# Kernel optimization log

Hardware: AMD Instinct MI355X
Metric: run time of the kernel (lower is better)

## Reference

```python
import math
import jax, jax.numpy as jnp
import numpy as np

EMBED_DIM = 1024
N_HEADS = 16
HEAD_DIM = EMBED_DIM // N_HEADS
B, T = 4, 2048


def setup_inputs() -> dict:
    key = jax.random.key(0)
    k1, k2, k3 = jax.random.split(key, 3)
    scale_in = 1.0 / math.sqrt(EMBED_DIM)
    return {
        "x": jax.random.normal(k1, (B, T, EMBED_DIM), dtype=jnp.float32),
        "direction": 0,  # 0=FORWARD (causal), 1=RETRODICTION (anti-causal), 2=CORRECTION (causal)
        "qkv_w": jax.random.normal(k2, (EMBED_DIM, 3 * EMBED_DIM), dtype=jnp.float32) * scale_in,
        "qkv_b": jnp.zeros((3 * EMBED_DIM,), dtype=jnp.float32),
        "proj_w": jax.random.normal(k3, (EMBED_DIM, EMBED_DIM), dtype=jnp.float32) * scale_in,
        "proj_b": jnp.zeros((EMBED_DIM,), dtype=jnp.float32),
    }


def reference(x, direction, qkv_w, qkv_b, proj_w, proj_b):
    Bx, Tx, C = x.shape
    qkv = x @ qkv_w + qkv_b                        # [B,T,3C]
    q, k, v = jnp.split(qkv, 3, axis=-1)
    # [B,T,C] -> [B,H,T,D]
    def heads(t):
        return t.reshape(Bx, Tx, N_HEADS, HEAD_DIM).transpose(0, 2, 1, 3)
    q, k, v = heads(q), heads(k), heads(v)
    scale = 1.0 / math.sqrt(HEAD_DIM)
    attn = jnp.einsum('bhqd,bhkd->bhqk', q, k) * scale
    rows = jnp.arange(Tx)[:, None]
    cols = jnp.arange(Tx)[None, :]
    if direction == 1:  # RETRODICTION -> anti-causal (upper triangular allowed)
        mask = cols >= rows
    else:               # FORWARD / CORRECTION -> causal
        mask = cols <= rows
    attn = jnp.where(mask[None, None], attn, -jnp.inf)
    attn = jax.nn.softmax(attn, axis=-1)  # dropout p=0 -> identity
    out = jnp.einsum('bhqk,bhkd->bhqd', attn, v)   # [B,H,T,D]
    out = out.transpose(0, 2, 1, 3).reshape(Bx, Tx, C)
    return out @ proj_w + proj_b
```

## Files before the change

### kernel.cpp

```cpp
#include <hip/hip_runtime.h>
#include <math.h>

typedef __bf16 bf16_t;
typedef bf16_t bf16x8 __attribute__((ext_vector_type(8)));
typedef bf16_t bf16x4 __attribute__((ext_vector_type(4)));
typedef float  f32x4  __attribute__((ext_vector_type(4)));
typedef float  floatv4 __attribute__((ext_vector_type(4)));

#define AS1 __attribute__((address_space(1)))
#define AS3 __attribute__((address_space(3)))

static __device__ __forceinline__ void gld_lds16(const void* g, void* l) {
  __builtin_amdgcn_global_load_lds((const AS1 unsigned int*)g,
                                   (AS3 unsigned int*)l, 16, 0, 0);
}
static __device__ __forceinline__ void block_sync() {
  asm volatile("" ::: "memory");
  __builtin_amdgcn_s_barrier();
  asm volatile("" ::: "memory");
}

__global__ __launch_bounds__(256) void k_cast(const float* __restrict__ in,
                                              bf16_t* __restrict__ out, int n4) {
  int i = blockIdx.x * 256 + threadIdx.x;
  if (i >= n4) return;
  floatv4 v = ((const floatv4*)in)[i];
  bf16x4 o;
  o.x = (bf16_t)v.x; o.y = (bf16_t)v.y; o.z = (bf16_t)v.z; o.w = (bf16_t)v.w;
  ((bf16x4*)out)[i] = o;
}

__global__ __launch_bounds__(256) void k_transpose_cast(const float* __restrict__ in,
                                                        bf16_t* __restrict__ out,
                                                        int R, int Cc) {
  __shared__ float tile[32][33];
  int c0 = blockIdx.x * 32, r0 = blockIdx.y * 32;
  int tx = threadIdx.x, ty = threadIdx.y;
#pragma unroll
  for (int i = 0; i < 32; i += 8)
    tile[ty + i][tx] = in[(size_t)(r0 + ty + i) * Cc + c0 + tx];
  __syncthreads();
#pragma unroll
  for (int i = 0; i < 32; i += 8)
    out[(size_t)(c0 + ty + i) * R + r0 + tx] = (bf16_t)tile[tx][ty + i];
}

__global__ __launch_bounds__(512, 2) void k_gemm_qkv(
    const bf16_t* __restrict__ A, const bf16_t* __restrict__ Bt,
    const float* __restrict__ bias,
    bf16_t* __restrict__ qo, bf16_t* __restrict__ ko, bf16_t* __restrict__ vto) {
  const int K = 1024;
  __shared__ __align__(16) char smem[122880];
  const int m0 = blockIdx.x * 256, n0 = blockIdx.y * 384;
  const int t = threadIdx.x, lane = t & 63, wv = t >> 6;
  const int ln15 = lane & 15, lhi = lane >> 4;
  const int wr = wv >> 2, wc = wv & 3;

  f32x4 acc[8][6];
#pragma unroll
  for (int m = 0; m < 8; ++m)
#pragma unroll
    for (int n = 0; n < 6; ++n) acc[m][n] = (f32x4){0.f, 0.f, 0.f, 0.f};
  bf16x8 af[4], bfr[6];

  const bf16_t* aS = A + (size_t)(m0 + wv * 16 + ln15) * K + lhi * 8;
  const bf16_t* bS = Bt + (size_t)(n0 + wv * 16 + ln15) * K + lhi * 8;
  const int dA = wv * 1024 + lane * 16;

  auto stageA = [&](int k0, char* buf) {
    gld_lds16(aS + k0, buf + dA);
    gld_lds16(aS + (size_t)128 * K + k0, buf + 8192 + dA);
  };
  auto stageB = [&](int k0, char* buf) {
    gld_lds16(bS + k0, buf + 16384 + dA);
    gld_lds16(bS + (size_t)128 * K + k0, buf + 24576 + dA);
    gld_lds16(bS + (size_t)256 * K + k0, buf + 32768 + dA);
  };

  char* b0 = smem;
  char* b1 = smem + 40960;
  char* b2 = smem + 81920;
  stageA(0, b0); stageB(0, b0);
  stageA(32, b1); stageB(32, b1);
  asm volatile("s_waitcnt vmcnt(5)" ::: "memory");
  block_sync();

#pragma unroll 1
  for (int it = 0; it < 32; ++it) {
    const bool st = (it + 2 < 32);
    const int k0n = (it + 2) * 32;
#pragma unroll
    for (int m = 0; m < 4; ++m)
      af[m] = *(const bf16x8*)(b0 + (wr * 8 + m) * 1024 + lane * 16);
#pragma unroll
    for (int n = 0; n < 6; ++n)
      bfr[n] = *(const bf16x8*)(b0 + 16384 + (wc * 6 + n) * 1024 + lane * 16);
    if (st) stageA(k0n, b2);
    block_sync();
    asm volatile("s_waitcnt lgkmcnt(0)" ::: "memory");
    __builtin_amdgcn_sched_barrier(0);
    __builtin_amdgcn_s_setprio(1);
#pragma unroll
    for (int m = 0; m < 4; ++m)
#pragma unroll
      for (int n = 0; n < 6; ++n)
        acc[m][n] = __builtin_amdgcn_mfma_f32_16x16x32_bf16(af[m], bfr[n], acc[m][n], 0, 0, 0);
    __builtin_amdgcn_s_setprio(0);
    block_sync();
#pragma unroll
    for (int m = 0; m < 4; ++m)
      af[m] = *(const bf16x8*)(b0 + (wr * 8 + 4 + m) * 1024 + lane * 16);
    if (st) stageB(k0n, b2);
    block_sync();
    asm volatile("s_waitcnt lgkmcnt(0)" ::: "memory");
    __builtin_amdgcn_sched_barrier(0);
    __builtin_amdgcn_s_setprio(1);
#pragma unroll
    for (int m = 0; m < 4; ++m)
#pragma unroll
      for (int n = 0; n < 6; ++n)
        acc[4 + m][n] = __builtin_amdgcn_mfma_f32_16x16x32_bf16(af[m], bfr[n], acc[4 + m][n], 0, 0, 0);
    __builtin_amdgcn_s_setprio(0);
    if (st) asm volatile("s_waitcnt vmcnt(5)" ::: "memory");
    else if (it + 1 < 32) asm volatile("s_waitcnt vmcnt(0)" ::: "memory");
    block_sync();
    char* tmp = b0; b0 = b1; b1 = b2; b2 = tmp;
  }

  bf16_t* L = (bf16_t*)smem;
  const int bq = m0 >> 11, ttb = m0 & 2047;
#pragma unroll 1
  for (int p = 0; p < 3; ++p) {
    const int wcol0 = n0 + p * 128;
    const int which = wcol0 >> 10;
    const float bscale = (which == 0) ? 0.18033688011112042f : 1.0f;
#pragma unroll
    for (int n = 0; n < 6; ++n) {
      const int c16 = wc * 6 + n;
      if ((c16 >> 3) == p) {
        const int colL = c16 * 16 - p * 128 + ln15;
        const float bv = bias[n0 + c16 * 16 + ln15];
#pragma unroll
        for (int m = 0; m < 8; ++m)
#pragma unroll
          for (int j = 0; j < 4; ++j) {
            const int row = wr * 128 + m * 16 + lhi * 4 + j;
            const bf16_t ob = (bf16_t)((acc[m][n][j] + bv) * bscale);
            if (which == 2) L[colL * 264 + row] = ob;
            else            L[row * 132 + colL] = ob;
          }
      }
    }
    block_sync();
    if (which == 2) {
#pragma unroll
      for (int c = 0; c < 8; ++c) {
        const int idx = c * 512 + t;
        const int vcol = idx >> 5, r8 = (idx & 31) * 8;
        bf16x8 v8 = *(const bf16x8*)&L[vcol * 264 + r8];
        const int cc = (wcol0 & 1023) + vcol;
        const int hh = cc >> 6, d = cc & 63;
        *(bf16x8*)&vto[((size_t)(bq * 16 + hh) * 64 + d) * 2048 + ttb + r8] = v8;
      }
    } else {
      bf16_t* dst = (which == 0) ? qo : ko;
#pragma unroll
      for (int c = 0; c < 8; ++c) {
        const int idx = c * 512 + t;
        const int row = idx >> 4, c8 = (idx & 15) * 8;
        bf16x8 v8 = *(const bf16x8*)&L[row * 132 + c8];
        const int cc = (wcol0 & 1023) + c8;
        const int hh = cc >> 6, d = cc & 63;
        *(bf16x8*)&dst[((size_t)(bq * 16 + hh) * 2048 + ttb + row) * 64 + d] = v8;
      }
    }
    block_sync();
  }
}

__global__ __launch_bounds__(256) void k_attn4(
    const bf16_t* __restrict__ q, const bf16_t* __restrict__ k,
    const bf16_t* __restrict__ vt, const int* __restrict__ dirp,
    bf16_t* __restrict__ a2) {
  const int T = 2048;
  __shared__ __align__(16) bf16_t smem[16384];
  const int bh = blockIdx.x, b = bh >> 4, h = bh & 15;
  const int jb = blockIdx.y;
  const int t = threadIdx.x, lane = t & 63, wv = t >> 6;
  const int ln15 = lane & 15, lhi = lane >> 4;
  const bool anti = (*dirp == 1);

  const bf16_t* kbase = k + (size_t)bh * T * 64;
  const bf16_t* vbase = vt + (size_t)bh * 64 * T;

  auto stage = [&](int kc0, int buf) {
    char* Kd = (char*)smem + buf * 16384;
    char* Vd = Kd + 8192;
#pragma unroll
    for (int s = 0; s < 2; ++s) {
      const int qk = s * 4 + wv;
      const int krow = kc0 + (qk >> 2) * 32 + ((qk >> 1) & 1) * 4 +
                       ((lane & 15) >> 2) * 8 + (lane & 3);
      const int kcolb = (lane >> 4) * 16 + (qk & 1) * 64;
      gld_lds16((const char*)kbase + (size_t)krow * 128 + kcolb,
                Kd + s * 4096 + t * 16);
      const int vd = (qk & 3) * 16 + (lane & 15);
      gld_lds16((const char*)vbase + (size_t)vd * 4096 + (size_t)kc0 * 2 +
                    (qk >> 2) * 64 + (lane >> 4) * 16,
                Vd + s * 4096 + t * 16);
    }
  };

#pragma unroll 1
  for (int sel = 0; sel < 2; ++sel) {
    const int qt = sel ? (15 - jb) : jb;
    const int q0w = qt * 128 + wv * 32;

    bf16x8 qf[2][2];
#pragma unroll
    for (int g = 0; g < 2; ++g) {
      const bf16_t* qp = q + ((size_t)bh * T + q0w + g * 16 + ln15) * 64 + lhi * 8;
      qf[g][0] = *(const bf16x8*)qp;
      qf[g][1] = *(const bf16x8*)(qp + 32);
    }

    f32x4 acc[2][4];
#pragma unroll
    for (int g = 0; g < 2; ++g)
#pragma unroll
      for (int dg = 0; dg < 4; ++dg) acc[g][dg] = (f32x4){0.f, 0.f, 0.f, 0.f};
    float mrun[2] = {-3.0e38f, -3.0e38f}, lrun[2] = {0.f, 0.f};

    const int kt0 = anti ? 2 * qt : 0;
    const int nb  = anti ? (32 - 2 * qt) : (2 * qt + 2);

    stage(kt0 * 64, 0);
#pragma unroll 1
    for (int i = 0; i < nb; ++i) {
      const int kt = kt0 + i;
      const int buf = i & 1;
      if (i + 1 < nb) {
        stage((kt + 1) * 64, buf ^ 1);
        asm volatile("s_waitcnt vmcnt(4)" ::: "memory");
      } else {
        asm volatile("s_waitcnt vmcnt(0)" ::: "memory");
      }
      block_sync();
      const bf16_t* Kb = smem + buf * 8192;
      const bf16_t* Vb = Kb + 4096;

      const bool active = anti ? (kt * 64 + 63 >= q0w) : (kt * 64 <= q0w + 31);
      if (active) {
        float sc[2][16];
#pragma unroll
        for (int kh = 0; kh < 2; ++kh) {
          bf16x8 kf0 = *(const bf16x8*)(Kb + (kh * 4 + 0) * 512 + lane * 8);
          bf16x8 kf1 = *(const bf16x8*)(Kb + (kh * 4 + 1) * 512 + lane * 8);
          bf16x8 kf2 = *(const bf16x8*)(Kb + (kh * 4 + 2) * 512 + lane * 8);
          bf16x8 kf3 = *(const bf16x8*)(Kb + (kh * 4 + 3) * 512 + lane * 8);
#pragma unroll
          for (int g = 0; g < 2; ++g) {
            const f32x4 zz = (f32x4){0.f, 0.f, 0.f, 0.f};
            f32x4 slo = __builtin_amdgcn_mfma_f32_16x16x32_bf16(kf0, qf[g][0], zz, 0, 0, 0);
            slo = __builtin_amdgcn_mfma_f32_16x16x32_bf16(kf1, qf[g][1], slo, 0, 0, 0);
            f32x4 shi = __builtin_amdgcn_mfma_f32_16x16x32_bf16(kf2, qf[g][0], zz, 0, 0, 0);
            shi = __builtin_amdgcn_mfma_f32_16x16x32_bf16(kf3, qf[g][1], shi, 0, 0, 0);
#pragma unroll
            for (int j = 0; j < 4; ++j) {
              sc[g][kh * 8 + j] = slo[j];
              sc[g][kh * 8 + 4 + j] = shi[j];
            }
          }
        }
        bf16x8 vfr[8];
#pragma unroll
        for (int dg = 0; dg < 8; ++dg)
          vfr[dg] = *(const bf16x8*)(Vb + dg * 512 + lane * 8);
#pragma unroll
        for (int g = 0; g < 2; ++g) {
          const int grow = q0w + g * 16 + ln15;
          const bool needm = anti ? (kt * 64 < q0w + g * 16 + 15)
                                  : (kt * 64 + 63 > q0w + g * 16);
          if (needm) {
#pragma unroll
            for (int e = 0; e < 16; ++e) {
              const int col = kt * 64 + (e >> 3) * 32 + lhi * 8 + (e & 7);
              const bool ok = anti ? (col >= grow) : (col <= grow);
              sc[g][e] = ok ? sc[g][e] : -3.0e38f;
            }
          }
          float lmax = sc[g][0];
#pragma unroll
          for (int e = 1; e < 16; ++e) lmax = fmaxf(lmax, sc[g][e]);
          if (!__all(lmax <= mrun[g] + 8.f)) {
            float vm = lmax;
            vm = fmaxf(vm, __shfl_xor(vm, 16));
            vm = fmaxf(vm, __shfl_xor(vm, 32));
            const float mn = fmaxf(mrun[g], vm);
            const float al = __builtin_amdgcn_exp2f(mrun[g] - mn);
            lrun[g] *= al;
#pragma unroll
            for (int dg = 0; dg < 4; ++dg) acc[g][dg] *= al;
            mrun[g] = mn;
          }
          bf16x8 pb0, pb1;
          float rs = 0.f;
#pragma unroll
          for (int e = 0; e < 8; ++e) {
            float p = __builtin_amdgcn_exp2f(sc[g][e] - mrun[g]);
            rs += p; pb0[e] = (bf16_t)p;
          }
#pragma unroll
          for (int e = 0; e < 8; ++e) {
            float p = __builtin_amdgcn_exp2f(sc[g][8 + e] - mrun[g]);
            rs += p; pb1[e] = (bf16_t)p;
          }
          lrun[g] += rs;
#pragma unroll
          for (int dg = 0; dg < 4; ++dg)
            acc[g][dg] = __builtin_amdgcn_mfma_f32_16x16x32_bf16(vfr[dg], pb0, acc[g][dg], 0, 0, 0);
#pragma unroll
          for (int dg = 0; dg < 4; ++dg)
            acc[g][dg] = __builtin_amdgcn_mfma_f32_16x16x32_bf16(vfr[4 + dg], pb1, acc[g][dg], 0, 0, 0);
        }
      }
      block_sync();
    }

#pragma unroll
    for (int g = 0; g < 2; ++g) {
      float l = lrun[g];
      l += __shfl_xor(l, 16);
      l += __shfl_xor(l, 32);
      const float inv = __builtin_amdgcn_rcpf(l);
      bf16_t* op = a2 + ((size_t)b * T + q0w + g * 16 + ln15) * 1024 + h * 64 + lhi * 4;
#pragma unroll
      for (int dg = 0; dg < 4; ++dg) {
        bf16x4 o4;
#pragma unroll
        for (int jx = 0; jx < 4; ++jx) o4[jx] = (bf16_t)(acc[g][dg][jx] * inv);
        *(bf16x4*)(op + dg * 16) = o4;
      }
    }
  }
}

__global__ __launch_bounds__(512, 2) void k_gemm_proj(
    const bf16_t* __restrict__ A, const bf16_t* __restrict__ Bt,
    const float* __restrict__ bias, float* __restrict__ out) {
  const int K = 1024;
  __shared__ __align__(16) char smem[73728];
  const int m0 = blockIdx.x * 256, n0 = blockIdx.y * 128;
  const int t = threadIdx.x, lane = t & 63, wv = t >> 6;
  const int ln15 = lane & 15, lhi = lane >> 4;
  const int wr = wv >> 2, wc = wv & 3;

  f32x4 acc[8][2];
#pragma unroll
  for (int m = 0; m < 8; ++m)
#pragma unroll
    for (int n = 0; n < 2; ++n) acc[m][n] = (f32x4){0.f, 0.f, 0.f, 0.f};
  bf16x8 af[4], bfr[2];

  const bf16_t* aS = A + (size_t)(m0 + wv * 16 + ln15) * K + lhi * 8;
  const bf16_t* bS = Bt + (size_t)(n0 + wv * 16 + ln15) * K + lhi * 8;
  const int dA = wv * 1024 + lane * 16;

  auto stageA = [&](int k0, char* buf) {
    gld_lds16(aS + k0, buf + dA);
    gld_lds16(aS + (size_t)128 * K + k0, buf + 8192 + dA);
  };
  auto stageB = [&](int k0, char* buf) {
    gld_lds16(bS + k0, buf + 16384 + dA);
  };

  char* b0 = smem;
  char* b1 = smem + 24576;
  char* b2 = smem + 49152;
  stageA(0, b0); stageB(0, b0);
  stageA(32, b1); stageB(32, b1);
  asm volatile("s_waitcnt vmcnt(3)" ::: "memory");
  block_sync();

#pragma unroll 1
  for (int it = 0; it < 32; ++it) {
    const bool st = (it + 2 < 32);
    const int k0n = (it + 2) * 32;
#pragma unroll
    for (int m = 0; m < 4; ++m)
      af[m] = *(const bf16x8*)(b0 + (wr * 8 + m) * 1024 + lane * 16);
#pragma unroll
    for (int n = 0; n < 2; ++n)
      bfr[n] = *(const bf16x8*)(b0 + 16384 + (wc * 2 + n) * 1024 + lane * 16);
    if (st) stageA(k0n, b2);
    block_sync();
    asm volatile("s_waitcnt lgkmcnt(0)" ::: "memory");
    __builtin_amdgcn_sched_barrier(0);
    __builtin_amdgcn_s_setprio(1);
#pragma unroll
    for (int m = 0; m < 4; ++m)
#pragma unroll
      for (int n = 0; n < 2; ++n)
        acc[m][n] = __builtin_amdgcn_mfma_f32_16x16x32_bf16(af[m], bfr[n], acc[m][n], 0, 0, 0);
    __builtin_amdgcn_s_setprio(0);
    block_sync();
#pragma unroll
    for (int m = 0; m < 4; ++m)
      af[m] = *(const bf16x8*)(b0 + (wr * 8 + 4 + m) * 1024 + lane * 16);
    if (st) stageB(k0n, b2);
    block_sync();
    asm volatile("s_waitcnt lgkmcnt(0)" ::: "memory");
    __builtin_amdgcn_sched_barrier(0);
    __builtin_amdgcn_s_setprio(1);
#pragma unroll
    for (int m = 0; m < 4; ++m)
#pragma unroll
      for (int n = 0; n < 2; ++n)
        acc[4 + m][n] = __builtin_amdgcn_mfma_f32_16x16x32_bf16(af[m], bfr[n], acc[4 + m][n], 0, 0, 0);
    __builtin_amdgcn_s_setprio(0);
    if (st) asm volatile("s_waitcnt vmcnt(3)" ::: "memory");
    else if (it + 1 < 32) asm volatile("s_waitcnt vmcnt(0)" ::: "memory");
    block_sync();
    char* tmp = b0; b0 = b1; b1 = b2; b2 = tmp;
  }

#pragma unroll
  for (int n = 0; n < 2; ++n) {
    const int col = n0 + wc * 32 + n * 16 + ln15;
    const float bv = bias[col];
#pragma unroll
    for (int m = 0; m < 8; ++m)
#pragma unroll
      for (int j = 0; j < 4; ++j) {
        const int row = m0 + wr * 128 + m * 16 + lhi * 4 + j;
        out[(size_t)row * 1024 + col] = acc[m][n][j] + bv;
      }
  }
}

extern "C" void kernel_launch(void* const* d_in, const int* in_sizes, int n_in,
                              void* d_out, int out_size, void* d_ws, size_t ws_size,
                              hipStream_t stream) {
  (void)in_sizes; (void)n_in; (void)out_size; (void)ws_size;
  const float* x      = (const float*)d_in[0];
  const int*   dirp   = (const int*)d_in[1];
  const float* qkv_w  = (const float*)d_in[2];
  const float* qkv_b  = (const float*)d_in[3];
  const float* proj_w = (const float*)d_in[4];
  const float* proj_b = (const float*)d_in[5];
  float* out = (float*)d_out;

  char* ws = (char*)d_ws;
  bf16_t* xb   = (bf16_t*)(ws);
  bf16_t* wq_t = (bf16_t*)(ws + 16777216);
  bf16_t* wp_t = (bf16_t*)(ws + 23068672);
  bf16_t* qb   = (bf16_t*)(ws + 25165824);
  bf16_t* kb   = (bf16_t*)(ws + 41943040);
  bf16_t* vtb  = (bf16_t*)(ws + 58720256);
  bf16_t* a2   = xb;

  k_cast<<<8192, 256, 0, stream>>>(x, xb, 2097152);
  k_transpose_cast<<<dim3(96, 32), dim3(32, 8), 0, stream>>>(qkv_w, wq_t, 1024, 3072);
  k_transpose_cast<<<dim3(32, 32), dim3(32, 8), 0, stream>>>(proj_w, wp_t, 1024, 1024);
  k_gemm_qkv<<<dim3(32, 8), 512, 0, stream>>>(xb, wq_t, qkv_b, qb, kb, vtb);
  k_attn4<<<dim3(64, 8), 256, 0, stream>>>(qb, kb, vtb, dirp, a2);
  k_gemm_proj<<<dim3(32, 8), 512, 0, stream>>>(a2, wp_t, proj_b, out);
}
```

Measured before the change: 193.1 us.

## Replace LDS-staged GEMM pipelines with direct global-to-register double-buffered MFMA loops

Both the QKV and output-projection GEMMs drop their LDS-staged, triple-buffered pipelines and their barrier-heavy main loops. Each wave now loads its A and B fragments straight from global memory into registers, double-buffered, and computes a 64x64 subtile. The QKV GEMM tile shrinks from 256x384 to 256x128, which triples the grid and simplifies the epilogue to a single output pass. The goal is to remove barrier and LDS overhead and to raise parallelism, at the cost of relying on L1/L2 caches for reuse across waves and of less coalesced strided global loads.

Result: slower. 332.0 us (+71.9%).

```diff
diff --git a/kernel.cpp b/kernel.cpp
--- a/kernel.cpp
+++ b/kernel.cpp
@@ -50,131 +50,87 @@
     const float* __restrict__ bias,
     bf16_t* __restrict__ qo, bf16_t* __restrict__ ko, bf16_t* __restrict__ vto) {
   const int K = 1024;
-  __shared__ __align__(16) char smem[122880];
-  const int m0 = blockIdx.x * 256, n0 = blockIdx.y * 384;
+  __shared__ __align__(16) char smem[67584];
+  const int m0 = blockIdx.x * 256, n0 = blockIdx.y * 128;
   const int t = threadIdx.x, lane = t & 63, wv = t >> 6;
   const int ln15 = lane & 15, lhi = lane >> 4;
-  const int wr = wv >> 2, wc = wv & 3;
-
-  f32x4 acc[8][6];
-#pragma unroll
-  for (int m = 0; m < 8; ++m)
-#pragma unroll
-    for (int n = 0; n < 6; ++n) acc[m][n] = (f32x4){0.f, 0.f, 0.f, 0.f};
-  bf16x8 af[4], bfr[6];
-
-  const bf16_t* aS = A + (size_t)(m0 + wv * 16 + ln15) * K + lhi * 8;
-  const bf16_t* bS = Bt + (size_t)(n0 + wv * 16 + ln15) * K + lhi * 8;
-  const int dA = wv * 1024 + lane * 16;
-
-  auto stageA = [&](int k0, char* buf) {
-    gld_lds16(aS + k0, buf + dA);
-    gld_lds16(aS + (size_t)128 * K + k0, buf + 8192 + dA);
-  };
-  auto stageB = [&](int k0, char* buf) {
-    gld_lds16(bS + k0, buf + 16384 + dA);
-    gld_lds16(bS + (size_t)128 * K + k0, buf + 24576 + dA);
-    gld_lds16(bS + (size_t)256 * K + k0, buf + 32768 + dA);
-  };
-
-  char* b0 = smem;
-  char* b1 = smem + 40960;
-  char* b2 = smem + 81920;
-  stageA(0, b0); stageB(0, b0);
-  stageA(32, b1); stageB(32, b1);
-  asm volatile("s_waitcnt vmcnt(5)" ::: "memory");
+  const int wr = wv >> 1, wc = wv & 1;
+
+  f32x4 acc[4][4];
+#pragma unroll
+  for (int m = 0; m < 4; ++m)
+#pragma unroll
+    for (int n = 0; n < 4; ++n) acc[m][n] = (f32x4){0.f, 0.f, 0.f, 0.f};
+
+  const bf16_t* aP = A + (size_t)(m0 + wr * 64 + ln15) * K + lhi * 8;
+  const bf16_t* bP = Bt + (size_t)(n0 + wc * 64 + ln15) * K + lhi * 8;
+
+  auto LD = [&](bf16x8 af[4], bf16x8 bf[4], int k0) {
+#pragma unroll
+    for (int m = 0; m < 4; ++m)
+      af[m] = *(const bf16x8*)(aP + (size_t)m * 16 * K + k0);
+#pragma unroll
+    for (int n = 0; n < 4; ++n)
+      bf[n] = *(const bf16x8*)(bP + (size_t)n * 16 * K + k0);
+  };
+  auto FM = [&](const bf16x8 af[4], const bf16x8 bf[4]) {
+#pragma unroll
+    for (int m = 0; m < 4; ++m)
+#pragma unroll
+      for (int n = 0; n < 4; ++n)
+        acc[m][n] = __builtin_amdgcn_mfma_f32_16x16x32_bf16(af[m], bf[n], acc[m][n], 0, 0, 0);
+  };
+
+  bf16x8 a0[4], b0[4], a1[4], b1[4];
+  LD(a0, b0, 0);
+#pragma unroll 1
+  for (int k0 = 0; k0 < K; k0 += 64) {
+    LD(a1, b1, k0 + 32);
+    FM(a0, b0);
+    if (k0 + 64 < K) LD(a0, b0, k0 + 64);
+    FM(a1, b1);
+  }
+
+  const int which = n0 >> 10;
+  const float bscale = (which == 0) ? 0.18033688011112042f : 1.0f;
+  bf16_t* L = (bf16_t*)smem;
+#pragma unroll
+  for (int n = 0; n < 4; ++n) {
+    const int col = wc * 64 + n * 16 + ln15;
+    const float bv = bias[n0 + col];
+#pragma unroll
+    for (int m = 0; m < 4; ++m)
+#pragma unroll
+      for (int j = 0; j < 4; ++j) {
+        const int row = wr * 64 + m * 16 + lhi * 4 + j;
+        const bf16_t ob = (bf16_t)((acc[m][n][j] + bv) * bscale);
+        if (which == 2) L[col * 264 + row] = ob;
+        else            L[row * 132 + col] = ob;
+      }
+  }
   block_sync();
-
-#pragma unroll 1
-  for (int it = 0; it < 32; ++it) {
-    const bool st = (it + 2 < 32);
-    const int k0n = (it + 2) * 32;
-#pragma unroll
-    for (int m = 0; m < 4; ++m)
-      af[m] = *(const bf16x8*)(b0 + (wr * 8 + m) * 1024 + lane * 16);
-#pragma unroll
-    for (int n = 0; n < 6; ++n)
-      bfr[n] = *(const bf16x8*)(b0 + 16384 + (wc * 6 + n) * 1024 + lane * 16);
-    if (st) stageA(k0n, b2);
-    block_sync();
-    asm volatile("s_waitcnt lgkmcnt(0)" ::: "memory");
-    __builtin_amdgcn_sched_barrier(0);
-    __builtin_amdgcn_s_setprio(1);
-#pragma unroll
-    for (int m = 0; m < 4; ++m)
-#pragma unroll
-      for (int n = 0; n < 6; ++n)
-        acc[m][n] = __builtin_amdgcn_mfma_f32_16x16x32_bf16(af[m], bfr[n], acc[m][n], 0, 0, 0);
-    __builtin_amdgcn_s_setprio(0);
-    block_sync();
-#pragma unroll
-    for (int m = 0; m < 4; ++m)
-      af[m] = *(const bf16x8*)(b0 + (wr * 8 + 4 + m) * 1024 + lane * 16);
-    if (st) stageB(k0n, b2);
-    block_sync();
-    asm volatile("s_waitcnt lgkmcnt(0)" ::: "memory");
-    __builtin_amdgcn_sched_barrier(0);
-    __builtin_amdgcn_s_setprio(1);
-#pragma unroll
-    for (int m = 0; m < 4; ++m)
-#pragma unroll
-      for (int n = 0; n < 6; ++n)
-        acc[4 + m][n] = __builtin_amdgcn_mfma_f32_16x16x32_bf16(af[m], bfr[n], acc[4 + m][n], 0, 0, 0);
-    __builtin_amdgcn_s_setprio(0);
-    if (st) asm volatile("s_waitcnt vmcnt(5)" ::: "memory");
-    else if (it + 1 < 32) asm volatile("s_waitcnt vmcnt(0)" ::: "memory");
-    block_sync();
-    char* tmp = b0; b0 = b1; b1 = b2; b2 = tmp;
-  }
-
-  bf16_t* L = (bf16_t*)smem;
   const int bq = m0 >> 11, ttb = m0 & 2047;
-#pragma unroll 1
-  for (int p = 0; p < 3; ++p) {
-    const int wcol0 = n0 + p * 128;
-    const int which = wcol0 >> 10;
-    const float bscale = (which == 0) ? 0.18033688011112042f : 1.0f;
-#pragma unroll
-    for (int n = 0; n < 6; ++n) {
-      const int c16 = wc * 6 + n;
-      if ((c16 >> 3) == p) {
-        const int colL = c16 * 16 - p * 128 + ln15;
-        const float bv = bias[n0 + c16 * 16 + ln15];
-#pragma unroll
-        for (int m = 0; m < 8; ++m)
-#pragma unroll
-          for (int j = 0; j < 4; ++j) {
-            const int row = wr * 128 + m * 16 + lhi * 4 + j;
-            const bf16_t ob = (bf16_t)((acc[m][n][j] + bv) * bscale);
-            if (which == 2) L[colL * 264 + row] = ob;
-            else            L[row * 132 + colL] = ob;
-          }
-      }
-    }
-    block_sync();
-    if (which == 2) {
-#pragma unroll
-      for (int c = 0; c < 8; ++c) {
-        const int idx = c * 512 + t;
-        const int vcol = idx >> 5, r8 = (idx & 31) * 8;
-        bf16x8 v8 = *(const bf16x8*)&L[vcol * 264 + r8];
-        const int cc = (wcol0 & 1023) + vcol;
-        const int hh = cc >> 6, d = cc & 63;
-        *(bf16x8*)&vto[((size_t)(bq * 16 + hh) * 64 + d) * 2048 + ttb + r8] = v8;
-      }
-    } else {
-      bf16_t* dst = (which == 0) ? qo : ko;
-#pragma unroll
-      for (int c = 0; c < 8; ++c) {
-        const int idx = c * 512 + t;
-        const int row = idx >> 4, c8 = (idx & 15) * 8;
-        bf16x8 v8 = *(const bf16x8*)&L[row * 132 + c8];
-        const int cc = (wcol0 & 1023) + c8;
-        const int hh = cc >> 6, d = cc & 63;
-        *(bf16x8*)&dst[((size_t)(bq * 16 + hh) * 2048 + ttb + row) * 64 + d] = v8;
-      }
-    }
-    block_sync();
+  if (which == 2) {
+#pragma unroll
+    for (int c = 0; c < 8; ++c) {
+      const int idx = c * 512 + t;
+      const int vcol = idx >> 5, r8 = (idx & 31) * 8;
+      bf16x8 v8 = *(const bf16x8*)&L[vcol * 264 + r8];
+      const int cc = (n0 + vcol) & 1023;
+      const int hh = cc >> 6, d = cc & 63;
+      *(bf16x8*)&vto[((size_t)(bq * 16 + hh) * 64 + d) * 2048 + ttb + r8] = v8;
+    }
+  } else {
+    bf16_t* dst = (which == 0) ? qo : ko;
+#pragma unroll
+    for (int c = 0; c < 8; ++c) {
+      const int idx = c * 512 + t;
+      const int row = idx >> 4, c8 = (idx & 15) * 8;
+      bf16x8 v8 = *(const bf16x8*)&L[row * 132 + c8];
+      const int cc = (n0 & 1023) + c8;
+      const int hh = cc >> 6, d = cc & 63;
+      *(bf16x8*)&dst[((size_t)(bq * 16 + hh) * 2048 + ttb + row) * 64 + d] = v8;
+    }
   }
 }
 
@@ -349,90 +305,55 @@
     const bf16_t* __restrict__ A, const bf16_t* __restrict__ Bt,
     const float* __restrict__ bias, float* __restrict__ out) {
   const int K = 1024;
-  __shared__ __align__(16) char smem[73728];
   const int m0 = blockIdx.x * 256, n0 = blockIdx.y * 128;
   const int t = threadIdx.x, lane = t & 63, wv = t >> 6;
   const int ln15 = lane & 15, lhi = lane >> 4;
-  const int wr = wv >> 2, wc = wv & 3;
-
-  f32x4 acc[8][2];
-#pragma unroll
-  for (int m = 0; m < 8; ++m)
-#pragma unroll
-    for (int n = 0; n < 2; ++n) acc[m][n] = (f32x4){0.f, 0.f, 0.f, 0.f};
-  bf16x8 af[4], bfr[2];
-
-  const bf16_t* aS = A + (size_t)(m0 + wv * 16 + ln15) * K + lhi * 8;
-  const bf16_t* bS = Bt + (size_t)(n0 + wv * 16 + ln15) * K + lhi * 8;
-  const int dA = wv * 1024 + lane * 16;
-
-  auto stageA = [&](int k0, char* buf) {
-    gld_lds16(aS + k0, buf + dA);
-    gld_lds16(aS + (size_t)128 * K + k0, buf + 8192 + dA);
-  };
-  auto stageB = [&](int k0, char* buf) {
-    gld_lds16(bS + k0, buf + 16384 + dA);
-  };
-
-  char* b0 = smem;
-  char* b1 = smem + 24576;
-  char* b2 = smem + 49152;
-  stageA(0, b0); stageB(0, b0);
-  stageA(32, b1); stageB(32, b1);
-  asm volatile("s_waitcnt vmcnt(3)" ::: "memory");
-  block_sync();
-
+  const int wr = wv >> 1, wc = wv & 1;
+
+  f32x4 acc[4][4];
+#pragma unroll
+  for (int m = 0; m < 4; ++m)
+#pragma unroll
+    for (int n = 0; n < 4; ++n) acc[m][n] = (f32x4){0.f, 0.f, 0.f, 0.f};
+
+  const bf16_t* aP = A + (size_t)(m0 + wr * 64 + ln15) * K + lhi * 8;
+  const bf16_t* bP = Bt + (size_t)(n0 + wc * 64 + ln15) * K + lhi * 8;
+
+  auto LD = [&](bf16x8 af[4], bf16x8 bf[4], int k0) {
+#pragma unroll
+    for (int m = 0; m < 4; ++m)
+      af[m] = *(const bf16x8*)(aP + (size_t)m * 16 * K + k0);
+#pragma unroll
+    for (int n = 0; n < 4; ++n)
+      bf[n] = *(const bf16x8*)(bP + (size_t)n * 16 * K + k0);
+  };
+  auto FM = [&](const bf16x8 af[4], const bf16x8 bf[4]) {
+#pragma unroll
+    for (int m = 0; m < 4; ++m)
+#pragma unroll
+      for (int n = 0; n < 4; ++n)
+        acc[m][n] = __builtin_amdgcn_mfma_f32_16x16x32_bf16(af[m], bf[n], acc[m][n], 0, 0, 0);
+  };
+
+  bf16x8 a0[4], b0[4], a1[4], b1[4];
+  LD(a0, b0, 0);
 #pragma unroll 1
-  for (int it = 0; it < 32; ++it) {
-    const bool st = (it + 2 < 32);
-    const int k0n = (it + 2) * 32;
-#pragma unroll
-    for (int m = 0; m < 4; ++m)
-      af[m] = *(const bf16x8*)(b0 + (wr * 8 + m) * 1024 + lane * 16);
-#pragma unroll
-    for (int n = 0; n < 2; ++n)
-      bfr[n] = *(const bf16x8*)(b0 + 16384 + (wc * 2 + n) * 1024 + lane * 16);
-    if (st) stageA(k0n, b2);
-    block_sync();
-    asm volatile("s_waitcnt lgkmcnt(0)" ::: "memory");
-    __builtin_amdgcn_sched_barrier(0);
-    __builtin_amdgcn_s_setprio(1);
-#pragma unroll
-    for (int m = 0; m < 4; ++m)
-#pragma unroll
-      for (int n = 0; n < 2; ++n)
-        acc[m][n] = __builtin_amdgcn_mfma_f32_16x16x32_bf16(af[m], bfr[n], acc[m][n], 0, 0, 0);
-    __builtin_amdgcn_s_setprio(0);
-    block_sync();
-#pragma unroll
-    for (int m = 0; m < 4; ++m)
-      af[m] = *(const bf16x8*)(b0 + (wr * 8 + 4 + m) * 1024 + lane * 16);
-    if (st) stageB(k0n, b2);
-    block_sync();
-    asm volatile("s_waitcnt lgkmcnt(0)" ::: "memory");
-    __builtin_amdgcn_sched_barrier(0);
-    __builtin_amdgcn_s_setprio(1);
-#pragma unroll
-    for (int m = 0; m < 4; ++m)
-#pragma unroll
-      for (int n = 0; n < 2; ++n)
-        acc[4 + m][n] = __builtin_amdgcn_mfma_f32_16x16x32_bf16(af[m], bfr[n], acc[4 + m][n], 0, 0, 0);
-    __builtin_amdgcn_s_setprio(0);
-    if (st) asm volatile("s_waitcnt vmcnt(3)" ::: "memory");
-    else if (it + 1 < 32) asm volatile("s_waitcnt vmcnt(0)" ::: "memory");
-    block_sync();
-    char* tmp = b0; b0 = b1; b1 = b2; b2 = tmp;
-  }
-
-#pragma unroll
-  for (int n = 0; n < 2; ++n) {
-    const int col = n0 + wc * 32 + n * 16 + ln15;
+  for (int k0 = 0; k0 < K; k0 += 64) {
+    LD(a1, b1, k0 + 32);
+    FM(a0, b0);
+    if (k0 + 64 < K) LD(a0, b0, k0 + 64);
+    FM(a1, b1);
+  }
+
+#pragma unroll
+  for (int n = 0; n < 4; ++n) {
+    const int col = n0 + wc * 64 + n * 16 + ln15;
     const float bv = bias[col];
 #pragma unroll
-    for (int m = 0; m < 8; ++m)
+    for (int m = 0; m < 4; ++m)
 #pragma unroll
       for (int j = 0; j < 4; ++j) {
-        const int row = m0 + wr * 128 + m * 16 + lhi * 4 + j;
+        const int row = m0 + wr * 64 + m * 16 + lhi * 4 + j;
         out[(size_t)row * 1024 + col] = acc[m][n][j] + bv;
       }
   }
@@ -462,7 +383,7 @@
   k_cast<<<8192, 256, 0, stream>>>(x, xb, 2097152);
   k_transpose_cast<<<dim3(96, 32), dim3(32, 8), 0, stream>>>(qkv_w, wq_t, 1024, 3072);
   k_transpose_cast<<<dim3(32, 32), dim3(32, 8), 0, stream>>>(proj_w, wp_t, 1024, 1024);
-  k_gemm_qkv<<<dim3(32, 8), 512, 0, stream>>>(xb, wq_t, qkv_b, qb, kb, vtb);
+  k_gemm_qkv<<<dim3(32, 24), 512, 0, stream>>>(xb, wq_t, qkv_b, qb, kb, vtb);
   k_attn4<<<dim3(64, 8), 256, 0, stream>>>(qb, kb, vtb, dirp, a2);
   k_gemm_proj<<<dim3(32, 8), 512, 0, stream>>>(a2, wp_t, proj_b, out);
 }
```
